# Kernel optimization log

Measured on AMD Instinct MI355X. Metric: run time of the kernel, lower is better.

Reference implementation:

```python
import jax, jax.numpy as jnp
import numpy as np

DIM = 1024
HEADS = 16
HEAD_DIM = DIM // HEADS
SCALE = HEAD_DIM ** -0.5


def setup_inputs() -> dict:
    key = jax.random.key(0)
    ks = jax.random.split(key, 7)
    B, N, M = 2, 2048, 2048
    x = jax.random.normal(ks[0], (B, N, DIM), dtype=jnp.float32)
    y = jax.random.normal(ks[1], (B, M, DIM), dtype=jnp.float32)
    s = DIM ** -0.5
    Wq = jax.random.normal(ks[2], (DIM, DIM), dtype=jnp.float32) * s
    Wk = jax.random.normal(ks[3], (DIM, DIM), dtype=jnp.float32) * s
    Wv = jax.random.normal(ks[4], (DIM, DIM), dtype=jnp.float32) * s
    Wp = jax.random.normal(ks[5], (DIM, DIM), dtype=jnp.float32) * s
    bp = jax.random.normal(ks[6], (DIM,), dtype=jnp.float32) * 0.01
    return {"x": x, "y": y, "Wq": Wq, "Wk": Wk, "Wv": Wv, "Wp": Wp, "bp": bp}


def _split_heads(t):
    b, n, _ = t.shape
    return t.reshape(b, n, HEADS, HEAD_DIM).transpose(0, 2, 1, 3)  # b h n d


def reference(x, y, Wq, Wk, Wv, Wp, bp):
    q = _split_heads(x @ Wq)  # [b,h,n,d]
    k = _split_heads(y @ Wk)  # [b,h,m,d]
    v = _split_heads(y @ Wv)  # [b,h,m,d]
    attn = jnp.einsum('bhid,bhjd->bhij', q, k) * SCALE  # [b,h,n,m]
    attn = jax.nn.softmax(attn, axis=-1)
    out = jnp.einsum('bhij,bhjd->bhid', attn, v)  # [b,h,n,d]
    b, h, n, d = out.shape
    out = out.transpose(0, 2, 1, 3).reshape(b, n, h * d)  # [b,n,dim]
    return out @ Wp + bp
```

## Files before the change

### kernel.cpp

```cpp
#include <hip/hip_runtime.h>
#include <hip/hip_bf16.h>
#include <cstdint>

#define DIM   1024
#define HEADS 16
#define HDIM  64
#define BATCH 2
#define SEQ   2048
#define ROWS  (BATCH*SEQ)
static constexpr float QSCALE = 0.18033688f;

typedef float  f32x4  __attribute__((ext_vector_type(4)));
typedef float  float4v __attribute__((ext_vector_type(4)));
typedef __bf16 bf16x8 __attribute__((ext_vector_type(8)));
typedef __bf16 bf16x4 __attribute__((ext_vector_type(4)));
typedef short  short4v __attribute__((ext_vector_type(4)));

#if __has_builtin(__builtin_amdgcn_mfma_f32_16x16x16_bf16)
__device__ __forceinline__ f32x4 mfma16(bf16x4 a, bf16x4 b, f32x4 c) {
  return __builtin_amdgcn_mfma_f32_16x16x16_bf16(a, b, c, 0, 0, 0);
}
#else
__device__ __forceinline__ f32x4 mfma16(bf16x4 a, bf16x4 b, f32x4 c) {
  return __builtin_amdgcn_mfma_f32_16x16x16bf16_1k(
      __builtin_bit_cast(short4v, a), __builtin_bit_cast(short4v, b), c, 0, 0, 0);
}
#endif

__device__ __forceinline__ void glds16(const __bf16* g, __bf16* l) {
  __builtin_amdgcn_global_load_lds(
      (const __attribute__((address_space(1))) void*)g,
      (__attribute__((address_space(3))) void*)l, 16, 0, 0);
}

__global__ __launch_bounds__(256) void prep_kernel(
    const float* __restrict__ x, const float* __restrict__ y,
    const float* __restrict__ Wq, const float* __restrict__ Wk,
    const float* __restrict__ Wv, const float* __restrict__ Wp,
    __bf16* __restrict__ xb, __bf16* __restrict__ yb, __bf16* __restrict__ Wt) {
  const int z = blockIdx.z, t = threadIdx.x;
  const size_t NEL = (size_t)ROWS * DIM;
  if (z < 8) {
    size_t idx = (((size_t)z * 1024 + blockIdx.x) * 256 + t) * 4;
    const float* s; __bf16* d;
    if (idx < NEL) { s = x + idx; d = xb + idx; }
    else           { s = y + (idx - NEL); d = yb + (idx - NEL); }
    const float4v v = *(const float4v*)s;
    bf16x4 o;
    o[0] = (__bf16)v[0]; o[1] = (__bf16)v[1]; o[2] = (__bf16)v[2]; o[3] = (__bf16)v[3];
    *(bf16x4*)d = o;
    return;
  }
  const int w = blockIdx.x >> 8, rem = blockIdx.x & 255;
  const float* W = (w == 0) ? Wq : (w == 1) ? Wk : (w == 2) ? Wv : Wp;
  __bf16* dst = Wt + (size_t)w * DIM * DIM;
  const int n0 = (rem & 15) * 64, k0 = (rem >> 4) * 64;
  __shared__ float T[64][65];
  const int col = t & 63, rw = t >> 6;
  #pragma unroll
  for (int p = 0; p < 16; ++p) {
    const int row = p * 4 + rw;
    T[row][col] = W[(size_t)(k0 + row) * DIM + n0 + col];
  }
  __syncthreads();
  #pragma unroll
  for (int p = 0; p < 16; ++p) {
    const int row = p * 4 + rw;
    dst[(size_t)(n0 + row) * DIM + k0 + col] = (__bf16)T[col][row];
  }
}

__global__ __launch_bounds__(256) void proj_kernel(
    const __bf16* __restrict__ xb, const __bf16* __restrict__ yb,
    const __bf16* __restrict__ Wt,
    __bf16* __restrict__ Qb, __bf16* __restrict__ Kb, __bf16* __restrict__ VT) {
  const int z = blockIdx.z;
  const __bf16* A = (z == 0) ? xb : yb;
  const __bf16* Bt = Wt + (size_t)z * DIM * DIM;

  __shared__ __bf16 S[2][128 * 64];
  __bf16* As = S[0];
  __bf16* Bs = S[1];

  const int t = threadIdx.x, lane = t & 63, wave = t >> 6;
  const int l15 = lane & 15, quad = lane >> 4;
  const int wm = wave & 1, wn = wave >> 1;
  const int rowBase = blockIdx.y * 128, colBase = blockIdx.x * 128;
  const int srow = lane >> 3;
  const int scol = ((lane & 7) ^ srow) * 8;

  f32x4 acc[4][4] = {};

  for (int kb = 0; kb < DIM; kb += 64) {
    __syncthreads();
    #pragma unroll
    for (int i = 0; i < 4; ++i) {
      const int c = wave * 4 + i;
      const int row = c * 8 + srow;
      glds16(&A[(size_t)(rowBase + row) * DIM + kb + scol], &As[c * 512]);
      glds16(&Bt[(size_t)(colBase + row) * DIM + kb + scol], &Bs[c * 512]);
    }
    __syncthreads();
    #pragma unroll
    for (int ks = 0; ks < 2; ++ks) {
      bf16x8 a[4], b[4];
      #pragma unroll
      for (int mi = 0; mi < 4; ++mi) {
        const int row = wm * 64 + mi * 16 + l15;
        a[mi] = *(const bf16x8*)&As[row * 64 + (((ks << 2) | quad) ^ (row & 7)) * 8];
      }
      #pragma unroll
      for (int ni = 0; ni < 4; ++ni) {
        const int row = wn * 64 + ni * 16 + l15;
        b[ni] = *(const bf16x8*)&Bs[row * 64 + (((ks << 2) | quad) ^ (row & 7)) * 8];
      }
      #pragma unroll
      for (int mi = 0; mi < 4; ++mi)
        #pragma unroll
        for (int ni = 0; ni < 4; ++ni)
          acc[mi][ni] = __builtin_amdgcn_mfma_f32_16x16x32_bf16(a[mi], b[ni], acc[mi][ni], 0, 0, 0);
    }
  }

  if (z < 2) {
    __bf16* out = (z == 0) ? Qb : Kb;
    const float sc = (z == 0) ? QSCALE : 1.0f;
    #pragma unroll
    for (int mi = 0; mi < 4; ++mi) {
      const int row0 = rowBase + wm * 64 + mi * 16 + quad * 4;
      #pragma unroll
      for (int ni = 0; ni < 4; ++ni) {
        const int col = colBase + wn * 64 + ni * 16 + l15;
        #pragma unroll
        for (int r = 0; r < 4; ++r)
          out[(size_t)(row0 + r) * DIM + col] = (__bf16)(acc[mi][ni][r] * sc);
      }
    }
    return;
  }

  __syncthreads();
  __bf16* Ts = &S[0][0];
  #pragma unroll
  for (int mi = 0; mi < 4; ++mi) {
    const int bk3 = wm * 8 + mi * 2 + (quad >> 1);
    #pragma unroll
    for (int ni = 0; ni < 4; ++ni) {
      const int dl = wn * 64 + ni * 16 + l15;
      bf16x4 pk;
      #pragma unroll
      for (int r = 0; r < 4; ++r) pk[r] = (__bf16)acc[mi][ni][r];
      *(bf16x4*)&Ts[dl * 128 + (bk3 ^ (dl & 7)) * 8 + (quad & 1) * 4] = pk;
    }
  }
  __syncthreads();
  const int d = t >> 1, khh = t & 1;
  const size_t vrow = (size_t)((rowBase >> 11) * HEADS * HDIM) + colBase + d;
  const int key0g = rowBase & (SEQ - 1);
  #pragma unroll
  for (int j = 0; j < 8; ++j) {
    const int kc = khh * 8 + j;
    const int lc = (kc & 8) | ((kc ^ d) & 7);
    const bf16x8 v = *(const bf16x8*)&Ts[d * 128 + lc * 8];
    *(bf16x8*)&VT[vrow * SEQ + key0g + kc * 8] = v;
  }
}

__global__ __launch_bounds__(256, 2) void attn_kernel(
    const __bf16* __restrict__ Qb, const __bf16* __restrict__ Kb,
    const __bf16* __restrict__ VT, __bf16* __restrict__ Ob) {
  __shared__ __bf16 KV[2][2][64 * 64];
  __shared__ float lb[2][128];

  const int t = threadIdx.x, lane = t & 63, wave = t >> 6;
  const int l15 = lane & 15, quad = lane >> 4;
  const int bh = blockIdx.y, b = bh >> 4, h = bh & 15;
  const int qseg = wave & 1, kh = wave >> 1;
  const int qrow0 = blockIdx.x * 128 + qseg * 64;
  const int srow = lane >> 3;
  const int scol = ((lane & 7) ^ srow) * 8;

  const __bf16* Kbh = Kb + (size_t)b * SEQ * DIM + h * HDIM;
  const __bf16* Vbh = VT + (size_t)bh * HDIM * SEQ;

  bf16x8 qf[4][2];
  #pragma unroll
  for (int mi = 0; mi < 4; ++mi)
    #pragma unroll
    for (int ks = 0; ks < 2; ++ks)
      qf[mi][ks] = *(const bf16x8*)&Qb[(size_t)(b * SEQ + qrow0 + mi * 16 + l15) * DIM
                                       + h * HDIM + ks * 32 + quad * 8];

  bf16x4 ones4;
  #pragma unroll
  for (int i = 0; i < 4; ++i) ones4[i] = (__bf16)1.0f;

  f32x4 o[4][4] = {};
  f32x4 lacc[4] = {};

  auto stage = [&](int jb, int buf) {
    #pragma unroll
    for (int i = 0; i < 2; ++i) {
      const int c = wave * 2 + i;
      const int row = c * 8 + srow;
      glds16(&Kbh[(size_t)(jb + row) * DIM + scol], &KV[buf][0][c * 512]);
      glds16(&Vbh[(size_t)row * SEQ + jb + scol], &KV[buf][1][c * 512]);
    }
  };

  stage(0, 0);
  for (int j = 0; j < SEQ / 64; ++j) {
    const int buf = j & 1;
    __syncthreads();
    if (j + 1 < SEQ / 64) stage((j + 1) * 64, buf ^ 1);
    const __bf16* Ks = KV[buf][0];
    const __bf16* Vs = KV[buf][1];

    f32x4 sT[2][4] = {};
    #pragma unroll
    for (int ks = 0; ks < 2; ++ks)
      #pragma unroll
      for (int ni = 0; ni < 2; ++ni) {
        const int key = kh * 32 + ni * 16 + l15;
        const bf16x8 kf = *(const bf16x8*)&Ks[key * 64 + (((ks << 2) | quad) ^ (key & 7)) * 8];
        #pragma unroll
        for (int mi = 0; mi < 4; ++mi)
          sT[ni][mi] = __builtin_amdgcn_mfma_f32_16x16x32_bf16(kf, qf[mi][ks], sT[ni][mi], 0, 0, 0);
      }

    bf16x4 pa[2][4];
    #pragma unroll
    for (int ni = 0; ni < 2; ++ni)
      #pragma unroll
      for (int mi = 0; mi < 4; ++mi)
        #pragma unroll
        for (int r = 0; r < 4; ++r)
          pa[ni][mi][r] = (__bf16)__builtin_amdgcn_exp2f(sT[ni][mi][r]);

    #pragma unroll
    for (int ni = 0; ni < 2; ++ni) {
      const int key0 = kh * 32 + ni * 16;
      #pragma unroll
      for (int mi = 0; mi < 4; ++mi)
        lacc[mi] = mfma16(pa[ni][mi], ones4, lacc[mi]);
      #pragma unroll
      for (int dt = 0; dt < 4; ++dt) {
        const int d = dt * 16 + l15;
        const bf16x4 vf = *(const bf16x4*)&Vs[d * 64
            + (((key0 >> 3) + (quad >> 1)) ^ (d & 7)) * 8 + (quad & 1) * 4];
        #pragma unroll
        for (int mi = 0; mi < 4; ++mi)
          o[mi][dt] = mfma16(pa[ni][mi], vf, o[mi][dt]);
      }
    }
  }

  __syncthreads();
  float* mb = (float*)&KV[0][0][0];
  if (l15 == 0) {
    #pragma unroll
    for (int mi = 0; mi < 4; ++mi)
      #pragma unroll
      for (int r = 0; r < 4; ++r)
        lb[kh][qseg * 64 + mi * 16 + quad * 4 + r] = lacc[mi][r];
  }
  if (kh == 1) {
    #pragma unroll
    for (int mi = 0; mi < 4; ++mi)
      #pragma unroll
      for (int r = 0; r < 4; ++r) {
        const int q = mi * 16 + quad * 4 + r;
        #pragma unroll
        for (int dt = 0; dt < 4; ++dt)
          mb[qseg * 4096 + q * 64 + dt * 16 + l15] = o[mi][dt][r];
      }
  }
  __syncthreads();
  if (kh == 0) {
    #pragma unroll
    for (int mi = 0; mi < 4; ++mi)
      #pragma unroll
      for (int r = 0; r < 4; ++r) {
        const int q = mi * 16 + quad * 4 + r;
        const float inv = 1.f / (lb[0][qseg * 64 + q] + lb[1][qseg * 64 + q]);
        const size_t row = (size_t)(b * SEQ + qrow0 + q);
        #pragma unroll
        for (int dt = 0; dt < 4; ++dt) {
          const float ov = o[mi][dt][r] + mb[qseg * 4096 + q * 64 + dt * 16 + l15];
          Ob[row * DIM + h * HDIM + dt * 16 + l15] = (__bf16)(ov * inv);
        }
      }
  }
}

__global__ __launch_bounds__(256) void outproj_kernel(
    const __bf16* __restrict__ A, const __bf16* __restrict__ Bt,
    const float* __restrict__ bias, float* __restrict__ out) {
  __shared__ __bf16 As[64 * 64];
  __shared__ __bf16 Bs[128 * 64];

  const int t = threadIdx.x, lane = t & 63, wave = t >> 6;
  const int l15 = lane & 15, quad = lane >> 4;
  const int wm = wave & 1, wn = wave >> 1;
  const int rowBase = blockIdx.y * 64, colBase = blockIdx.x * 128;
  const int srow = lane >> 3;
  const int scol = ((lane & 7) ^ srow) * 8;

  f32x4 acc[2][4] = {};

  for (int kb = 0; kb < DIM; kb += 64) {
    __syncthreads();
    #pragma unroll
    for (int i = 0; i < 2; ++i) {
      const int c = wave * 2 + i;
      const int row = c * 8 + srow;
      glds16(&A[(size_t)(rowBase + row) * DIM + kb + scol], &As[c * 512]);
    }
    #pragma unroll
    for (int i = 0; i < 4; ++i) {
      const int c = wave * 4 + i;
      const int row = c * 8 + srow;
      glds16(&Bt[(size_t)(colBase + row) * DIM + kb + scol], &Bs[c * 512]);
    }
    __syncthreads();
    #pragma unroll
    for (int ks = 0; ks < 2; ++ks) {
      bf16x8 a[2], b[4];
      #pragma unroll
      for (int mi = 0; mi < 2; ++mi) {
        const int row = wm * 32 + mi * 16 + l15;
        a[mi] = *(const bf16x8*)&As[row * 64 + (((ks << 2) | quad) ^ (row & 7)) * 8];
      }
      #pragma unroll
      for (int ni = 0; ni < 4; ++ni) {
        const int row = wn * 64 + ni * 16 + l15;
        b[ni] = *(const bf16x8*)&Bs[row * 64 + (((ks << 2) | quad) ^ (row & 7)) * 8];
      }
      #pragma unroll
      for (int mi = 0; mi < 2; ++mi)
        #pragma unroll
        for (int ni = 0; ni < 4; ++ni)
          acc[mi][ni] = __builtin_amdgcn_mfma_f32_16x16x32_bf16(a[mi], b[ni], acc[mi][ni], 0, 0, 0);
    }
  }

  #pragma unroll
  for (int mi = 0; mi < 2; ++mi) {
    const int row0 = rowBase + wm * 32 + mi * 16 + quad * 4;
    #pragma unroll
    for (int ni = 0; ni < 4; ++ni) {
      const int col = colBase + wn * 64 + ni * 16 + l15;
      const float bb = bias[col];
      #pragma unroll
      for (int r = 0; r < 4; ++r)
        out[(size_t)(row0 + r) * DIM + col] = acc[mi][ni][r] + bb;
    }
  }
}

extern "C" void kernel_launch(void* const* d_in, const int* in_sizes, int n_in,
                              void* d_out, int out_size, void* d_ws, size_t ws_size,
                              hipStream_t stream) {
  const float* x  = (const float*)d_in[0];
  const float* y  = (const float*)d_in[1];
  const float* Wq = (const float*)d_in[2];
  const float* Wk = (const float*)d_in[3];
  const float* Wv = (const float*)d_in[4];
  const float* Wp = (const float*)d_in[5];
  const float* bp = (const float*)d_in[6];
  float* out = (float*)d_out;

  const size_t NEL = (size_t)ROWS * DIM;
  __bf16* xb = (__bf16*)d_ws;
  __bf16* yb = xb + NEL;
  __bf16* Wt = yb + NEL;
  __bf16* Qb = Wt + NEL;
  __bf16* Kb = Qb + NEL;
  __bf16* VT = Kb + NEL;
  __bf16* Ob = xb;

  prep_kernel<<<dim3(1024, 1, 9), 256, 0, stream>>>(x, y, Wq, Wk, Wv, Wp, xb, yb, Wt);
  proj_kernel<<<dim3(DIM / 128, ROWS / 128, 3), 256, 0, stream>>>(xb, yb, Wt, Qb, Kb, VT);
  attn_kernel<<<dim3(SEQ / 128, BATCH * HEADS), 256, 0, stream>>>(Qb, Kb, VT, Ob);
  outproj_kernel<<<dim3(DIM / 128, ROWS / 64), 256, 0, stream>>>(Ob, Wt + 3 * NEL / 4, bp, out);
}
```

Before: 215.6 us.

## Rewrite attention inner loop with 32x32x16 MFMA and per-wave query ownership

The attention kernel now has each wave own 32 query rows across all 64 keys per tile, using 32x32x16 bf16 MFMAs for both QK^T and PV. This removes the split-key partial accumulators and the shared-memory merge at the end. The row sum is taken from the bf16-rounded probabilities in scalar registers instead of a ones-vector MFMA, and the P fragments are rearranged with permlane32_swap (shuffle fallback) so they feed the PV MFMA directly. An explicit vmcnt/lgkmcnt wait was added before the barrier for the async LDS loads. The cost is larger accumulator register use per wave and extra cross-lane permutes each tile.

```diff
diff --git a/kernel.cpp b/kernel.cpp
--- a/kernel.cpp
+++ b/kernel.cpp
@@ -11,26 +11,21 @@
 static constexpr float QSCALE = 0.18033688f;
 
 typedef float  f32x4  __attribute__((ext_vector_type(4)));
+typedef float  f32x16 __attribute__((ext_vector_type(16)));
 typedef float  float4v __attribute__((ext_vector_type(4)));
 typedef __bf16 bf16x8 __attribute__((ext_vector_type(8)));
 typedef __bf16 bf16x4 __attribute__((ext_vector_type(4)));
-typedef short  short4v __attribute__((ext_vector_type(4)));
-
-#if __has_builtin(__builtin_amdgcn_mfma_f32_16x16x16_bf16)
-__device__ __forceinline__ f32x4 mfma16(bf16x4 a, bf16x4 b, f32x4 c) {
-  return __builtin_amdgcn_mfma_f32_16x16x16_bf16(a, b, c, 0, 0, 0);
-}
-#else
-__device__ __forceinline__ f32x4 mfma16(bf16x4 a, bf16x4 b, f32x4 c) {
-  return __builtin_amdgcn_mfma_f32_16x16x16bf16_1k(
-      __builtin_bit_cast(short4v, a), __builtin_bit_cast(short4v, b), c, 0, 0, 0);
-}
-#endif
+typedef __bf16 bf16x2 __attribute__((ext_vector_type(2)));
+typedef unsigned u32x4v __attribute__((ext_vector_type(4)));
 
 __device__ __forceinline__ void glds16(const __bf16* g, __bf16* l) {
   __builtin_amdgcn_global_load_lds(
       (const __attribute__((address_space(1))) void*)g,
       (__attribute__((address_space(3))) void*)l, 16, 0, 0);
+}
+
+__device__ __forceinline__ void wait_dma0() {
+  asm volatile("s_waitcnt vmcnt(0) lgkmcnt(0)" ::: "memory");
 }
 
 __global__ __launch_bounds__(256) void prep_kernel(
@@ -170,33 +165,28 @@
     const __bf16* __restrict__ Qb, const __bf16* __restrict__ Kb,
     const __bf16* __restrict__ VT, __bf16* __restrict__ Ob) {
   __shared__ __bf16 KV[2][2][64 * 64];
-  __shared__ float lb[2][128];
 
   const int t = threadIdx.x, lane = t & 63, wave = t >> 6;
-  const int l15 = lane & 15, quad = lane >> 4;
+  const int x = lane & 31, hi = lane >> 5;
   const int bh = blockIdx.y, b = bh >> 4, h = bh & 15;
-  const int qseg = wave & 1, kh = wave >> 1;
-  const int qrow0 = blockIdx.x * 128 + qseg * 64;
+  const int qbase = blockIdx.x * 128 + wave * 32;
   const int srow = lane >> 3;
   const int scol = ((lane & 7) ^ srow) * 8;
 
   const __bf16* Kbh = Kb + (size_t)b * SEQ * DIM + h * HDIM;
   const __bf16* Vbh = VT + (size_t)bh * HDIM * SEQ;
 
-  bf16x8 qf[4][2];
-  #pragma unroll
-  for (int mi = 0; mi < 4; ++mi)
-    #pragma unroll
-    for (int ks = 0; ks < 2; ++ks)
-      qf[mi][ks] = *(const bf16x8*)&Qb[(size_t)(b * SEQ + qrow0 + mi * 16 + l15) * DIM
-                                       + h * HDIM + ks * 32 + quad * 8];
-
-  bf16x4 ones4;
-  #pragma unroll
-  for (int i = 0; i < 4; ++i) ones4[i] = (__bf16)1.0f;
-
-  f32x4 o[4][4] = {};
-  f32x4 lacc[4] = {};
+  bf16x8 qf[4];
+  #pragma unroll
+  for (int kd = 0; kd < 4; ++kd)
+    qf[kd] = *(const bf16x8*)&Qb[(size_t)(b * SEQ + qbase + x) * DIM
+                                 + h * HDIM + kd * 16 + hi * 8];
+
+  f32x16 o0 = {}, o1 = {};
+  float lsum = 0.f;
+
+  const int he16 = (hi ^ (x & 7)) << 4;
+  const int rowb = x * 128;
 
   auto stage = [&](int jb, int buf) {
     #pragma unroll
@@ -211,85 +201,81 @@
   stage(0, 0);
   for (int j = 0; j < SEQ / 64; ++j) {
     const int buf = j & 1;
+    wait_dma0();
     __syncthreads();
     if (j + 1 < SEQ / 64) stage((j + 1) * 64, buf ^ 1);
-    const __bf16* Ks = KV[buf][0];
-    const __bf16* Vs = KV[buf][1];
-
-    f32x4 sT[2][4] = {};
-    #pragma unroll
-    for (int ks = 0; ks < 2; ++ks)
-      #pragma unroll
-      for (int ni = 0; ni < 2; ++ni) {
-        const int key = kh * 32 + ni * 16 + l15;
-        const bf16x8 kf = *(const bf16x8*)&Ks[key * 64 + (((ks << 2) | quad) ^ (key & 7)) * 8];
-        #pragma unroll
-        for (int mi = 0; mi < 4; ++mi)
-          sT[ni][mi] = __builtin_amdgcn_mfma_f32_16x16x32_bf16(kf, qf[mi][ks], sT[ni][mi], 0, 0, 0);
-      }
-
-    bf16x4 pa[2][4];
-    #pragma unroll
-    for (int ni = 0; ni < 2; ++ni)
-      #pragma unroll
-      for (int mi = 0; mi < 4; ++mi)
-        #pragma unroll
-        for (int r = 0; r < 4; ++r)
-          pa[ni][mi][r] = (__bf16)__builtin_amdgcn_exp2f(sT[ni][mi][r]);
-
-    #pragma unroll
-    for (int ni = 0; ni < 2; ++ni) {
-      const int key0 = kh * 32 + ni * 16;
-      #pragma unroll
-      for (int mi = 0; mi < 4; ++mi)
-        lacc[mi] = mfma16(pa[ni][mi], ones4, lacc[mi]);
-      #pragma unroll
-      for (int dt = 0; dt < 4; ++dt) {
-        const int d = dt * 16 + l15;
-        const bf16x4 vf = *(const bf16x4*)&Vs[d * 64
-            + (((key0 >> 3) + (quad >> 1)) ^ (d & 7)) * 8 + (quad & 1) * 4];
-        #pragma unroll
-        for (int mi = 0; mi < 4; ++mi)
-          o[mi][dt] = mfma16(pa[ni][mi], vf, o[mi][dt]);
-      }
-    }
-  }
-
-  __syncthreads();
-  float* mb = (float*)&KV[0][0][0];
-  if (l15 == 0) {
-    #pragma unroll
-    for (int mi = 0; mi < 4; ++mi)
-      #pragma unroll
-      for (int r = 0; r < 4; ++r)
-        lb[kh][qseg * 64 + mi * 16 + quad * 4 + r] = lacc[mi][r];
-  }
-  if (kh == 1) {
-    #pragma unroll
-    for (int mi = 0; mi < 4; ++mi)
-      #pragma unroll
-      for (int r = 0; r < 4; ++r) {
-        const int q = mi * 16 + quad * 4 + r;
-        #pragma unroll
-        for (int dt = 0; dt < 4; ++dt)
-          mb[qseg * 4096 + q * 64 + dt * 16 + l15] = o[mi][dt][r];
-      }
-  }
-  __syncthreads();
-  if (kh == 0) {
-    #pragma unroll
-    for (int mi = 0; mi < 4; ++mi)
-      #pragma unroll
-      for (int r = 0; r < 4; ++r) {
-        const int q = mi * 16 + quad * 4 + r;
-        const float inv = 1.f / (lb[0][qseg * 64 + q] + lb[1][qseg * 64 + q]);
-        const size_t row = (size_t)(b * SEQ + qrow0 + q);
-        #pragma unroll
-        for (int dt = 0; dt < 4; ++dt) {
-          const float ov = o[mi][dt][r] + mb[qseg * 4096 + q * 64 + dt * 16 + l15];
-          Ob[row * DIM + h * HDIM + dt * 16 + l15] = (__bf16)(ov * inv);
-        }
-      }
+    const char* Ks = (const char*)KV[buf][0];
+    const char* Vs = (const char*)KV[buf][1];
+
+    f32x16 sT0 = {}, sT1 = {};
+    #pragma unroll
+    for (int kd = 0; kd < 4; ++kd) {
+      const bf16x8 kf = *(const bf16x8*)(Ks + rowb + (he16 ^ (kd << 5)));
+      sT0 = __builtin_amdgcn_mfma_f32_32x32x16_bf16(kf, qf[kd], sT0, 0, 0, 0);
+    }
+    #pragma unroll
+    for (int kd = 0; kd < 4; ++kd) {
+      const bf16x8 kf = *(const bf16x8*)(Ks + 4096 + rowb + (he16 ^ (kd << 5)));
+      sT1 = __builtin_amdgcn_mfma_f32_32x32x16_bf16(kf, qf[kd], sT1, 0, 0, 0);
+    }
+
+    #pragma unroll
+    for (int kt = 0; kt < 2; ++kt) {
+      const f32x16 s = kt ? sT1 : sT0;
+      unsigned w[8];
+      #pragma unroll
+      for (int i = 0; i < 8; ++i) {
+        const float p0 = __builtin_amdgcn_exp2f(s[2 * i]);
+        const float p1 = __builtin_amdgcn_exp2f(s[2 * i + 1]);
+        bf16x2 pk; pk[0] = (__bf16)p0; pk[1] = (__bf16)p1;
+        const unsigned u = __builtin_bit_cast(unsigned, pk);
+        w[i] = u;
+        lsum += __builtin_bit_cast(float, u << 16)
+              + __builtin_bit_cast(float, u & 0xffff0000u);
+      }
+#if __has_builtin(__builtin_amdgcn_permlane32_swap)
+      const auto s02 = __builtin_amdgcn_permlane32_swap(w[0], w[2], false, false);
+      const auto s13 = __builtin_amdgcn_permlane32_swap(w[1], w[3], false, false);
+      const auto s46 = __builtin_amdgcn_permlane32_swap(w[4], w[6], false, false);
+      const auto s57 = __builtin_amdgcn_permlane32_swap(w[5], w[7], false, false);
+      const u32x4v f0v = {(unsigned)s02[0], (unsigned)s13[0], (unsigned)s02[1], (unsigned)s13[1]};
+      const u32x4v f1v = {(unsigned)s46[0], (unsigned)s57[0], (unsigned)s46[1], (unsigned)s57[1]};
+#else
+      const unsigned q0 = __shfl_xor((int)w[0], 32, 64), q1 = __shfl_xor((int)w[1], 32, 64);
+      const unsigned q2 = __shfl_xor((int)w[2], 32, 64), q3 = __shfl_xor((int)w[3], 32, 64);
+      const unsigned q4 = __shfl_xor((int)w[4], 32, 64), q5 = __shfl_xor((int)w[5], 32, 64);
+      const unsigned q6 = __shfl_xor((int)w[6], 32, 64), q7 = __shfl_xor((int)w[7], 32, 64);
+      const u32x4v f0v = {hi ? q2 : w[0], hi ? q3 : w[1], hi ? w[2] : q0, hi ? w[3] : q1};
+      const u32x4v f1v = {hi ? q6 : w[4], hi ? q7 : w[5], hi ? w[6] : q4, hi ? w[7] : q5};
+#endif
+      const bf16x8 F0 = __builtin_bit_cast(bf16x8, f0v);
+      const bf16x8 F1 = __builtin_bit_cast(bf16x8, f1v);
+
+      const int kb0 = kt << 6;
+      {
+        const bf16x8 va = *(const bf16x8*)(Vs + rowb + (he16 ^ kb0));
+        const bf16x8 vb = *(const bf16x8*)(Vs + 4096 + rowb + (he16 ^ kb0));
+        o0 = __builtin_amdgcn_mfma_f32_32x32x16_bf16(F0, va, o0, 0, 0, 0);
+        o1 = __builtin_amdgcn_mfma_f32_32x32x16_bf16(F0, vb, o1, 0, 0, 0);
+      }
+      {
+        const bf16x8 va = *(const bf16x8*)(Vs + rowb + (he16 ^ (kb0 | 32)));
+        const bf16x8 vb = *(const bf16x8*)(Vs + 4096 + rowb + (he16 ^ (kb0 | 32)));
+        o0 = __builtin_amdgcn_mfma_f32_32x32x16_bf16(F1, va, o0, 0, 0, 0);
+        o1 = __builtin_amdgcn_mfma_f32_32x32x16_bf16(F1, vb, o1, 0, 0, 0);
+      }
+    }
+  }
+
+  const float ltot = lsum + __shfl_xor(lsum, 32, 64);
+  const float linv = 1.f / ltot;
+  #pragma unroll
+  for (int r = 0; r < 16; ++r) {
+    const int q = (r & 3) + 8 * (r >> 2) + 4 * hi;
+    const float inv = __shfl(linv, q, 64);
+    __bf16* dst = &Ob[(size_t)(b * SEQ + qbase + q) * DIM + h * HDIM + x];
+    dst[0]  = (__bf16)(o0[r] * inv);
+    dst[32] = (__bf16)(o1[r] * inv);
   }
 }
 
```

Result: faster. 208.8 us (-3.2%).
